# Kernel optimization log

Hardware: AMD Instinct MI355X
Metric: run time of the kernel (lower is better)

Reference implementation:

```python
import math
import jax, jax.numpy as jnp
import numpy as np

N_HEADS = 12
D_EMBED = 768
BATCH = 2
SEQ = 2048


def setup_inputs() -> dict:
    key = jax.random.key(0)
    ks = jax.random.split(key, 5)
    scale = 0.02
    return {
        "x": jax.random.normal(ks[0], (BATCH, SEQ, D_EMBED), dtype=jnp.float32),
        "w_in": jax.random.normal(ks[1], (D_EMBED, 3 * D_EMBED), dtype=jnp.float32) * scale,
        "b_in": jax.random.normal(ks[2], (3 * D_EMBED,), dtype=jnp.float32) * scale,
        "w_out": jax.random.normal(ks[3], (D_EMBED, D_EMBED), dtype=jnp.float32) * scale,
        "b_out": jax.random.normal(ks[4], (D_EMBED,), dtype=jnp.float32) * scale,
    }


def reference(x, w_in, b_in, w_out, b_out):
    # x: [B, S, D]
    B, S, D = x.shape
    H = N_HEADS
    dh = D // H
    # Fused QKV projection: [B, S, 3D]
    qkv = x @ w_in + b_in
    q, k, v = jnp.split(qkv, 3, axis=-1)
    # [B, S, D] -> [B, H, S, dh]
    def to_heads(t):
        return t.reshape(B, S, H, dh).transpose(0, 2, 1, 3)
    q, k, v = to_heads(q), to_heads(k), to_heads(v)
    # Scaled dot-product attention (non-causal, masked=False default)
    scale = 1.0 / math.sqrt(dh)
    scores = jnp.einsum("bhqd,bhkd->bhqk", q, k) * scale  # [B, H, S, S]
    probs = jax.nn.softmax(scores, axis=-1)
    out = jnp.einsum("bhqk,bhkd->bhqd", probs, v)  # [B, H, S, dh]
    # Merge heads: [B, S, D]
    out = out.transpose(0, 2, 1, 3).reshape(B, S, D)
    return out @ w_out + b_out
```

## Files before the change

### kernel.cpp

```cpp
#include <hip/hip_runtime.h>
#include <stdint.h>

#define B_   2
#define S_   2048
#define D_   768
#define H_   12
#define DH_  64
#define N3_  2304
#define M_   4096

typedef __attribute__((ext_vector_type(8))) short    bf16x8;
typedef __attribute__((ext_vector_type(4))) float    f32x4;
typedef __attribute__((ext_vector_type(4))) int      i32x4;
typedef __attribute__((ext_vector_type(4))) unsigned short u16x4;
typedef _Float16 f16x4 __attribute__((ext_vector_type(4)));
typedef __fp16   h16x2 __attribute__((ext_vector_type(2)));

#define KSCALE 0.18033688011112042f
#define LSTRIDE (24 * S_)
#define ONE_EL  ((size_t)24 * S_ * DH_)

__device__ inline unsigned short f2bf(float f) {
    union { float f; unsigned u; } v; v.f = f;
    unsigned r = v.u + 0x7FFFu + ((v.u >> 16) & 1u);
    return (unsigned short)(r >> 16);
}

__device__ inline void async_copy16(const void* g, void* l) {
    __builtin_amdgcn_global_load_lds((const __attribute__((address_space(1))) void*)g,
                                     (__attribute__((address_space(3))) void*)l, 16, 0, 0);
}

__global__ __launch_bounds__(256) void prep_all(
    const float* __restrict__ x, const float* __restrict__ w_in,
    const float* __restrict__ w_out,
    unsigned short* __restrict__ xb, unsigned short* __restrict__ winT,
    unsigned short* __restrict__ woutT)
{
    __shared__ unsigned short t[32][33];
    const int gid = blockIdx.x, tid = threadIdx.x;
    if (gid < 3072) {
        int i = gid * 256 + tid;
        f32x4 v = *(const f32x4*)(x + (size_t)i * 4);
        u16x4 o;
        o.x = f2bf(v.x); o.y = f2bf(v.y); o.z = f2bf(v.z); o.w = f2bf(v.w);
        *(u16x4*)(xb + (size_t)i * 4) = o;
        return;
    }
    const float* src; unsigned short* dst; int R, C, bx, by;
    if (gid < 4800) { int b = gid - 3072; src = w_in;  dst = winT;  R = D_; C = N3_; bx = b % 72; by = b / 72; }
    else            { int b = gid - 4800; src = w_out; dst = woutT; R = D_; C = D_;  bx = b % 24; by = b / 24; }
    int c0 = bx * 32, r0 = by * 32, tx = tid & 31, ty = tid >> 5;
#pragma unroll
    for (int j = 0; j < 4; j++)
        t[ty + j * 8][tx] = f2bf(src[(size_t)(r0 + ty + j * 8) * C + c0 + tx]);
    __syncthreads();
#pragma unroll
    for (int j = 0; j < 4; j++)
        dst[(size_t)(c0 + ty + j * 8) * R + r0 + tx] = t[tx][ty + j * 8];
}

__global__ __launch_bounds__(256) void gemm_qkv(
    const unsigned short* __restrict__ A,
    const unsigned short* __restrict__ Bt,
    const float* __restrict__ bias,
    unsigned short* __restrict__ QK,
    unsigned short* __restrict__ Vt)
{
    __shared__ __align__(16) short Al[128 * 32];
    __shared__ __align__(16) short Bl[96 * 32];

    const int tid  = threadIdx.x;
    const int w    = tid >> 6;
    const int lane = tid & 63;
    const int r    = lane & 15;
    const int quad = lane >> 4;
    const int m0   = blockIdx.y * 128;
    const int n0   = blockIdx.x * 96;
    const int wm   = (w & 1) * 64;
    const int wn   = (w >> 1) * 48;
    const int K    = D_;

    f32x4 acc[4][3];
#pragma unroll
    for (int i = 0; i < 4; i++)
#pragma unroll
        for (int j = 0; j < 3; j++) acc[i][j] = f32x4{0.f, 0.f, 0.f, 0.f};

    const int c0 = tid, c1 = tid + 256;
    const size_t ga0 = (size_t)(m0 + (c0 >> 2)) * K + (c0 & 3) * 8;
    const size_t ga1 = (size_t)(m0 + (c1 >> 2)) * K + (c1 & 3) * 8;
    const size_t gb0 = (size_t)(n0 + (c0 >> 2)) * K + (c0 & 3) * 8;
    const size_t gb1 = (size_t)(n0 + (c1 >> 2)) * K + (c1 & 3) * 8;
    short* lA0 = &Al[(0 * 256 + w * 64) * 8];
    short* lA1 = &Al[(1 * 256 + w * 64) * 8];
    short* lB0 = &Bl[(0 * 256 + w * 64) * 8];
    short* lB1 = &Bl[(1 * 256 + w * 64) * 8];

    for (int k0 = 0; k0 < K; k0 += 32) {
        __syncthreads();
        async_copy16(A  + ga0 + k0, lA0);
        async_copy16(A  + ga1 + k0, lA1);
        async_copy16(Bt + gb0 + k0, lB0);
        if (w < 2) async_copy16(Bt + gb1 + k0, lB1);
        __syncthreads();

        bf16x8 af[4], bf[3];
#pragma unroll
        for (int mi = 0; mi < 4; mi++)
            af[mi] = *(const bf16x8*)&Al[(wm + mi * 16 + r) * 32 + quad * 8];
#pragma unroll
        for (int ni = 0; ni < 3; ni++)
            bf[ni] = *(const bf16x8*)&Bl[(wn + ni * 16 + r) * 32 + quad * 8];
#pragma unroll
        for (int mi = 0; mi < 4; mi++)
#pragma unroll
            for (int ni = 0; ni < 3; ni++)
                acc[mi][ni] = __builtin_amdgcn_mfma_f32_16x16x32_bf16(
                    af[mi], bf[ni], acc[mi][ni], 0, 0, 0);
    }

    const size_t one = (size_t)B_ * H_ * S_ * DH_;
#pragma unroll
    for (int ni = 0; ni < 3; ni++) {
        int col  = n0 + wn + ni * 16 + r;
        float bv = bias[col];
        int part = col / 768;
        int cc   = col - part * 768;
        int h    = cc >> 6;
        int d    = cc & 63;
        if (part == 2) {
#pragma unroll
            for (int mi = 0; mi < 4; mi++) {
                int row0 = m0 + wm + mi * 16 + quad * 4;
                int b    = row0 >> 11;
                int s0   = row0 & 2047;
                u16x4 pk;
#pragma unroll
                for (int i = 0; i < 4; i++) {
                    union { _Float16 h; unsigned short s; } cv;
                    cv.h = (_Float16)(acc[mi][ni][i] + bv);
                    pk[i] = cv.s;
                }
                *(u16x4*)&Vt[(((size_t)(b * H_ + h)) * DH_ + d) * S_ + s0] = pk;
            }
        } else {
            float scl = (part == 1) ? KSCALE : 1.0f;
            unsigned short* dst = QK + (size_t)part * one;
#pragma unroll
            for (int mi = 0; mi < 4; mi++) {
#pragma unroll
                for (int i = 0; i < 4; i++) {
                    int row = m0 + wm + mi * 16 + quad * 4 + i;
                    int b   = row >> 11;
                    int s   = row & 2047;
                    dst[(((size_t)(b * H_ + h)) * S_ + s) * DH_ + d] =
                        f2bf((acc[mi][ni][i] + bv) * scl);
                }
            }
        }
    }
}

__global__ __launch_bounds__(256) void gemm_out(
    const unsigned short* __restrict__ A,
    const unsigned short* __restrict__ Bt,
    const float* __restrict__ bias,
    float* __restrict__ Cf)
{
    __shared__ __align__(16) short Al[64 * 32];
    __shared__ __align__(16) short Bl[64 * 32];

    const int tid  = threadIdx.x;
    const int w    = tid >> 6;
    const int lane = tid & 63;
    const int r    = lane & 15;
    const int quad = lane >> 4;
    const int m0   = blockIdx.y * 64;
    const int n0   = blockIdx.x * 64;
    const int wm   = (w & 1) * 32;
    const int wn   = (w >> 1) * 32;
    const int K    = D_;
    const int N    = D_;

    f32x4 acc[2][2];
#pragma unroll
    for (int i = 0; i < 2; i++)
#pragma unroll
        for (int j = 0; j < 2; j++) acc[i][j] = f32x4{0.f, 0.f, 0.f, 0.f};

    const size_t ga = (size_t)(m0 + (tid >> 2)) * K + (tid & 3) * 8;
    const size_t gb = (size_t)(n0 + (tid >> 2)) * K + (tid & 3) * 8;
    short* lA = &Al[(w * 64) * 8];
    short* lB = &Bl[(w * 64) * 8];

    for (int k0 = 0; k0 < K; k0 += 32) {
        __syncthreads();
        async_copy16(A  + ga + k0, lA);
        async_copy16(Bt + gb + k0, lB);
        __syncthreads();

        bf16x8 af[2], bf[2];
#pragma unroll
        for (int mi = 0; mi < 2; mi++)
            af[mi] = *(const bf16x8*)&Al[(wm + mi * 16 + r) * 32 + quad * 8];
#pragma unroll
        for (int ni = 0; ni < 2; ni++)
            bf[ni] = *(const bf16x8*)&Bl[(wn + ni * 16 + r) * 32 + quad * 8];
#pragma unroll
        for (int mi = 0; mi < 2; mi++)
#pragma unroll
            for (int ni = 0; ni < 2; ni++)
                acc[mi][ni] = __builtin_amdgcn_mfma_f32_16x16x32_bf16(
                    af[mi], bf[ni], acc[mi][ni], 0, 0, 0);
    }

#pragma unroll
    for (int ni = 0; ni < 2; ni++) {
        int col  = n0 + wn + ni * 16 + r;
        float bv = bias[col];
#pragma unroll
        for (int mi = 0; mi < 2; mi++) {
#pragma unroll
            for (int i = 0; i < 4; i++) {
                int row = m0 + wm + mi * 16 + quad * 4 + i;
                Cf[(size_t)row * N + col] = acc[mi][ni][i] + bv;
            }
        }
    }
}

__global__ __launch_bounds__(256) void attn_kernel(
    const unsigned short* __restrict__ Q,
    const unsigned short* __restrict__ K,
    const unsigned short* __restrict__ Vt,
    unsigned short* __restrict__ On,
    float* __restrict__ lbuf)
{
    __shared__ __align__(16) short Kl[64 * 64];
    __shared__ __align__(16) short Vl[64 * 64];

    const int tid  = threadIdx.x;
    const int w    = tid >> 6;
    const int lane = tid & 63;
    const int r    = lane & 15;
    const int quad = lane >> 4;
    const int xk   = r & 7;
    const int bid  = blockIdx.x;
    const int bh   = bid % 24;
    const int t2   = bid / 24;
    const int qb   = t2 & 15;
    const int quarter = t2 >> 4;
    const size_t baseQK = (size_t)bh * S_ * DH_;
    const size_t baseV  = (size_t)bh * DH_ * S_;
    const int q0   = qb * 128;
    const int kt0  = quarter * 8;

    bf16x8 qf[2][2];
#pragma unroll
    for (int qt = 0; qt < 2; qt++) {
        const unsigned short* qp =
            Q + baseQK + (size_t)(q0 + w * 32 + qt * 16 + r) * DH_ + quad * 8;
        qf[qt][0] = *(const bf16x8*)(qp);
        qf[qt][1] = *(const bf16x8*)(qp + 32);
    }

    f32x4 o[2][4];
    f32x4 lacc[2];
#pragma unroll
    for (int qt = 0; qt < 2; qt++) {
        lacc[qt] = f32x4{0.f, 0.f, 0.f, 0.f};
#pragma unroll
        for (int nb = 0; nb < 4; nb++) o[qt][nb] = f32x4{0.f, 0.f, 0.f, 0.f};
    }

    const f16x4 ONES = {(_Float16)1.f, (_Float16)1.f, (_Float16)1.f, (_Float16)1.f};

    const int srw = tid >> 3, schk = tid & 7;
    const unsigned short* kg = K  + baseQK + (size_t)kt0 * 4096 + tid * 8;
    const unsigned short* vg = Vt + baseV + (size_t)kt0 * 64 + (size_t)srw * S_ + schk * 8;
    const int lb = srw * 64 + (schk ^ (srw & 7)) * 8;

    i32x4 kreg[2], vreg[2];
    kreg[0] = *(const i32x4*)(kg);
    kreg[1] = *(const i32x4*)(kg + 2048);
    vreg[0] = *(const i32x4*)(vg);
    vreg[1] = *(const i32x4*)(vg + 32 * S_);

    for (int it = 0; it < 8; it++) {
        __syncthreads();
        *(i32x4*)&Kl[lb]        = kreg[0];
        *(i32x4*)&Kl[lb + 2048] = kreg[1];
        *(i32x4*)&Vl[lb]        = vreg[0];
        *(i32x4*)&Vl[lb + 2048] = vreg[1];
        __syncthreads();

        if (it != 7) {
            const unsigned short* kn = kg + (it + 1) * 4096;
            const unsigned short* vn = vg + (it + 1) * 64;
            kreg[0] = *(const i32x4*)(kn);
            kreg[1] = *(const i32x4*)(kn + 2048);
            vreg[0] = *(const i32x4*)(vn);
            vreg[1] = *(const i32x4*)(vn + 32 * S_);
        }

        f32x4 sa[2][4];
#pragma unroll
        for (int qt = 0; qt < 2; qt++)
#pragma unroll
            for (int kb = 0; kb < 4; kb++) sa[qt][kb] = f32x4{0.f, 0.f, 0.f, 0.f};
#pragma unroll
        for (int t = 0; t < 2; t++)
#pragma unroll
            for (int kb = 0; kb < 4; kb++) {
                bf16x8 kf = *(const bf16x8*)&Kl[(kb * 16 + r) * 64 + ((t * 4 + quad) ^ xk) * 8];
#pragma unroll
                for (int qt = 0; qt < 2; qt++)
                    sa[qt][kb] = __builtin_amdgcn_mfma_f32_16x16x32_bf16(
                        kf, qf[qt][t], sa[qt][kb], 0, 0, 0);
            }

        f16x4 pf[2][4];
#pragma unroll
        for (int qt = 0; qt < 2; qt++)
#pragma unroll
            for (int kb = 0; kb < 4; kb++) {
                float p0 = __builtin_amdgcn_exp2f(sa[qt][kb][0]);
                float p1 = __builtin_amdgcn_exp2f(sa[qt][kb][1]);
                float p2 = __builtin_amdgcn_exp2f(sa[qt][kb][2]);
                float p3 = __builtin_amdgcn_exp2f(sa[qt][kb][3]);
                union { f16x4 v; h16x2 h[2]; } u;
                u.h[0] = __builtin_amdgcn_cvt_pkrtz(p0, p1);
                u.h[1] = __builtin_amdgcn_cvt_pkrtz(p2, p3);
                pf[qt][kb] = u.v;
            }

#pragma unroll
        for (int kb = 0; kb < 4; kb++) {
#pragma unroll
            for (int nb = 0; nb < 4; nb++) {
                f16x4 vf = *(const f16x4*)&Vl[(nb * 16 + r) * 64 +
                                              ((kb * 2 + (quad >> 1)) ^ xk) * 8 + (quad & 1) * 4];
#pragma unroll
                for (int qt = 0; qt < 2; qt++)
                    o[qt][nb] = __builtin_amdgcn_mfma_f32_16x16x16f16(
                        pf[qt][kb], vf, o[qt][nb], 0, 0, 0);
            }
#pragma unroll
            for (int qt = 0; qt < 2; qt++)
                lacc[qt] = __builtin_amdgcn_mfma_f32_16x16x16f16(
                    pf[qt][kb], ONES, lacc[qt], 0, 0, 0);
        }
    }

    unsigned short* Ob = On + (size_t)quarter * ONE_EL;
#pragma unroll
    for (int qt = 0; qt < 2; qt++)
#pragma unroll
        for (int i = 0; i < 4; i++) {
            int s = q0 + w * 32 + qt * 16 + quad * 4 + i;
            size_t row = (size_t)bh * S_ + s;
            if (r == 0) lbuf[quarter * LSTRIDE + row] = lacc[qt][i];
#pragma unroll
            for (int nb = 0; nb < 4; nb++) {
                union { _Float16 h; unsigned short u; } cv;
                cv.h = (_Float16)o[qt][nb][i];
                Ob[row * 64 + nb * 16 + r] = cv.u;
            }
        }
}

__global__ void combine_attn(const unsigned short* __restrict__ On,
                             const float* __restrict__ lbuf,
                             unsigned short* __restrict__ Out)
{
    int g   = blockIdx.x * 256 + threadIdx.x;
    int hd8 = g % 96;
    int bs  = g / 96;
    int h   = hd8 >> 3;
    int d8  = (hd8 & 7) * 8;
    size_t row = ((size_t)((bs >> 11) * H_ + h)) * S_ + (bs & 2047);
    float inv = 1.0f / (lbuf[row] + lbuf[LSTRIDE + row] +
                        lbuf[2 * LSTRIDE + row] + lbuf[3 * LSTRIDE + row]);
    size_t ob = row * 64 + d8;
    i32x4 a0 = *(const i32x4*)&On[ob];
    i32x4 a1 = *(const i32x4*)&On[ob + ONE_EL];
    i32x4 a2 = *(const i32x4*)&On[ob + 2 * ONE_EL];
    i32x4 a3 = *(const i32x4*)&On[ob + 3 * ONE_EL];
    const _Float16* f0 = (const _Float16*)&a0;
    const _Float16* f1 = (const _Float16*)&a1;
    const _Float16* f2 = (const _Float16*)&a2;
    const _Float16* f3 = (const _Float16*)&a3;
    unsigned short tmp[8];
#pragma unroll
    for (int j = 0; j < 8; j++)
        tmp[j] = f2bf(((float)f0[j] + (float)f1[j] + (float)f2[j] + (float)f3[j]) * inv);
    *(i32x4*)&Out[(size_t)bs * D_ + h * 64 + d8] = *(const i32x4*)tmp;
}

extern "C" void kernel_launch(void* const* d_in, const int* in_sizes, int n_in,
                              void* d_out, int out_size, void* d_ws, size_t ws_size,
                              hipStream_t stream) {
    const float* x     = (const float*)d_in[0];
    const float* w_in  = (const float*)d_in[1];
    const float* b_in  = (const float*)d_in[2];
    const float* w_out = (const float*)d_in[3];
    const float* b_out = (const float*)d_in[4];
    float* out = (float*)d_out;
    char* ws = (char*)d_ws;

    unsigned short* xb    = (unsigned short*)(ws);
    unsigned short* winT  = (unsigned short*)(ws + 6291456);
    unsigned short* woutT = (unsigned short*)(ws + 9830400);
    unsigned short* QKV   = (unsigned short*)(ws + 11010048);
    unsigned short* On    = (unsigned short*)(ws + 36175872);

    const size_t one = (size_t)B_ * H_ * S_ * DH_;
    unsigned short* Vtbuf = QKV + 2 * one;
    float*          lbuf  = (float*)winT;
    unsigned short* attnO = QKV;

    prep_all<<<5376, 256, 0, stream>>>(x, w_in, w_out, xb, winT, woutT);

    gemm_qkv<<<dim3(N3_ / 96, M_ / 128), 256, 0, stream>>>(
        xb, winT, b_in, QKV, Vtbuf);

    attn_kernel<<<24 * 16 * 4, 256, 0, stream>>>(
        QKV, QKV + one, Vtbuf, On, lbuf);

    combine_attn<<<1536, 256, 0, stream>>>(On, lbuf, attnO);

    gemm_out<<<dim3(D_ / 64, M_ / 64), 256, 0, stream>>>(
        attnO, woutT, b_out, out);
}
```

Measured before the change: 159.9 us.

## Halve attention key splits and remap GEMM block order for L2 locality

The attention split-K factor drops from four key quarters to two halves, so each block walks 16 key tiles instead of 8. The combine kernel now reads and sums only two partial outputs and two row-sum buffers. Both GEMMs switch to a 1D grid with a swizzled mapping that groups 8 consecutive M tiles per N tile, to improve L2 reuse of the weight panels. The attention grid shrinks to 768 blocks, which cuts partial-result traffic but may reduce occupancy and parallelism on a GPU with many CUs.

```diff
diff --git a/kernel.cpp b/kernel.cpp
--- a/kernel.cpp
+++ b/kernel.cpp
@@ -75,8 +75,10 @@
     const int lane = tid & 63;
     const int r    = lane & 15;
     const int quad = lane >> 4;
-    const int m0   = blockIdx.y * 128;
-    const int n0   = blockIdx.x * 96;
+    const int bid  = blockIdx.x;
+    const int rest = bid >> 3;
+    const int m0   = ((bid & 7) + 8 * (rest / 24)) * 128;
+    const int n0   = (rest % 24) * 96;
     const int wm   = (w & 1) * 64;
     const int wn   = (w >> 1) * 48;
     const int K    = D_;
@@ -176,8 +178,10 @@
     const int lane = tid & 63;
     const int r    = lane & 15;
     const int quad = lane >> 4;
-    const int m0   = blockIdx.y * 64;
-    const int n0   = blockIdx.x * 64;
+    const int bid  = blockIdx.x;
+    const int rest = bid >> 3;
+    const int m0   = ((bid & 7) + 8 * (rest / 12)) * 64;
+    const int n0   = (rest % 12) * 64;
     const int wm   = (w & 1) * 32;
     const int wn   = (w >> 1) * 32;
     const int K    = D_;
@@ -250,11 +254,11 @@
     const int bh   = bid % 24;
     const int t2   = bid / 24;
     const int qb   = t2 & 15;
-    const int quarter = t2 >> 4;
+    const int half = t2 >> 4;
     const size_t baseQK = (size_t)bh * S_ * DH_;
     const size_t baseV  = (size_t)bh * DH_ * S_;
     const int q0   = qb * 128;
-    const int kt0  = quarter * 8;
+    const int kt0  = half * 16;
 
     bf16x8 qf[2][2];
 #pragma unroll
@@ -287,7 +291,7 @@
     vreg[0] = *(const i32x4*)(vg);
     vreg[1] = *(const i32x4*)(vg + 32 * S_);
 
-    for (int it = 0; it < 8; it++) {
+    for (int it = 0; it < 16; it++) {
         __syncthreads();
         *(i32x4*)&Kl[lb]        = kreg[0];
         *(i32x4*)&Kl[lb + 2048] = kreg[1];
@@ -295,7 +299,7 @@
         *(i32x4*)&Vl[lb + 2048] = vreg[1];
         __syncthreads();
 
-        if (it != 7) {
+        if (it != 15) {
             const unsigned short* kn = kg + (it + 1) * 4096;
             const unsigned short* vn = vg + (it + 1) * 64;
             kreg[0] = *(const i32x4*)(kn);
@@ -353,14 +357,14 @@
         }
     }
 
-    unsigned short* Ob = On + (size_t)quarter * ONE_EL;
+    unsigned short* Ob = On + (size_t)half * ONE_EL;
 #pragma unroll
     for (int qt = 0; qt < 2; qt++)
 #pragma unroll
         for (int i = 0; i < 4; i++) {
             int s = q0 + w * 32 + qt * 16 + quad * 4 + i;
             size_t row = (size_t)bh * S_ + s;
-            if (r == 0) lbuf[quarter * LSTRIDE + row] = lacc[qt][i];
+            if (r == 0) lbuf[half * LSTRIDE + row] = lacc[qt][i];
 #pragma unroll
             for (int nb = 0; nb < 4; nb++) {
                 union { _Float16 h; unsigned short u; } cv;
@@ -380,21 +384,16 @@
     int h   = hd8 >> 3;
     int d8  = (hd8 & 7) * 8;
     size_t row = ((size_t)((bs >> 11) * H_ + h)) * S_ + (bs & 2047);
-    float inv = 1.0f / (lbuf[row] + lbuf[LSTRIDE + row] +
-                        lbuf[2 * LSTRIDE + row] + lbuf[3 * LSTRIDE + row]);
+    float inv = 1.0f / (lbuf[row] + lbuf[LSTRIDE + row]);
     size_t ob = row * 64 + d8;
     i32x4 a0 = *(const i32x4*)&On[ob];
     i32x4 a1 = *(const i32x4*)&On[ob + ONE_EL];
-    i32x4 a2 = *(const i32x4*)&On[ob + 2 * ONE_EL];
-    i32x4 a3 = *(const i32x4*)&On[ob + 3 * ONE_EL];
     const _Float16* f0 = (const _Float16*)&a0;
     const _Float16* f1 = (const _Float16*)&a1;
-    const _Float16* f2 = (const _Float16*)&a2;
-    const _Float16* f3 = (const _Float16*)&a3;
     unsigned short tmp[8];
 #pragma unroll
     for (int j = 0; j < 8; j++)
-        tmp[j] = f2bf(((float)f0[j] + (float)f1[j] + (float)f2[j] + (float)f3[j]) * inv);
+        tmp[j] = f2bf(((float)f0[j] + (float)f1[j]) * inv);
     *(i32x4*)&Out[(size_t)bs * D_ + h * 64 + d8] = *(const i32x4*)tmp;
 }
 
@@ -422,14 +421,12 @@
 
     prep_all<<<5376, 256, 0, stream>>>(x, w_in, w_out, xb, winT, woutT);
 
-    gemm_qkv<<<dim3(N3_ / 96, M_ / 128), 256, 0, stream>>>(
-        xb, winT, b_in, QKV, Vtbuf);
-
-    attn_kernel<<<24 * 16 * 4, 256, 0, stream>>>(
+    gemm_qkv<<<768, 256, 0, stream>>>(xb, winT, b_in, QKV, Vtbuf);
+
+    attn_kernel<<<24 * 16 * 2, 256, 0, stream>>>(
         QKV, QKV + one, Vtbuf, On, lbuf);
 
     combine_attn<<<1536, 256, 0, stream>>>(On, lbuf, attnO);
 
-    gemm_out<<<dim3(D_ / 64, M_ / 64), 256, 0, stream>>>(
-        attnO, woutT, b_out, out);
-}
+    gemm_out<<<768, 256, 0, stream>>>(attnO, woutT, b_out, out);
+}
```

Result: no change. 157.8 us (-1.3%).
